# Performance work log

Measured on AMD Instinct MI355X. Metric: run time of the kernel, lower is better.

Reference implementation:

```python
import jax, jax.numpy as jnp
import numpy as np

B, L, H, NH = 32, 512, 256, 4
DH = H // NH
EPS = 1e-12


def setup_inputs() -> dict:
    key = jax.random.key(0)
    ks = jax.random.split(key, 24)
    p = lambda k, shape: 0.02 * jax.random.normal(k, shape, dtype=jnp.float32)
    return {
        "input_tensor": jax.random.normal(ks[0], (B, L, H), dtype=jnp.float32),
        # sorted positive timestamps (seconds-like scale)
        "time_seq": jnp.sort(jax.random.uniform(ks[1], (B, L), dtype=jnp.float32) * 100.0, axis=-1),
        "attention_mask": jnp.zeros((B, 1, L, L), dtype=jnp.float32),
        "item_seq_len": jnp.clip(jax.random.randint(ks[2], (B,), 0, L), 2, L),
        "Wq": p(ks[3], (H, H)), "bq": jnp.zeros((H,), jnp.float32),
        "Wk": p(ks[4], (H, H)), "bk": jnp.zeros((H,), jnp.float32),
        "Wv": p(ks[5], (H, H)), "bv": jnp.zeros((H,), jnp.float32),
        "Wd": p(ks[6], (H, H)), "bd": jnp.zeros((H,), jnp.float32),
        "ln_g": jnp.ones((H,), jnp.float32), "ln_b": jnp.zeros((H,), jnp.float32),
        "Wtq": p(ks[7], (H, H)), "btq": jnp.zeros((H,), jnp.float32),
        "tw1": p(ks[8], (L, L)), "tb1": p(ks[9], (L, L)),
        "tow1": p(ks[10], (L, L)), "tow2": p(ks[11], (L, L)), "tob": p(ks[12], (L, L)),
        "Wt": p(ks[13], (1, 2 * H)), "bt": jnp.zeros((1,), jnp.float32),
    }


def reference(input_tensor, time_seq, attention_mask, item_seq_len,
              Wq, bq, Wk, bk, Wv, bv, Wd, bd, ln_g, ln_b,
              Wtq, btq, tw1, tb1, tow1, tow2, tob, Wt, bt):
    x = input_tensor  # (B, L, H)

    def heads(t):  # (B,L,H) -> (B,NH,L,DH)
        return t.reshape(B, L, NH, DH).transpose(0, 2, 1, 3)

    q = heads(x @ Wq.T + bq)
    k = heads(x @ Wk.T + bk)
    v = heads(x @ Wv.T + bv)

    scores = jnp.einsum('bhqd,bhkd->bhqk', q, k)  # (B,NH,L,L)

    # --- time decay gate ---
    tq = x @ Wtq.T + btq                                  # (B,L,H)
    time_query_key = jnp.tanh(jnp.einsum('bqh,bkh->bqk', tq, x))  # (B,L,L)
    diff = jnp.abs(time_seq[:, :, None] - time_seq[:, None, :])   # |t_i - t_j|
    decay = jnp.tanh(jnp.log1p(diff) * tw1 + tb1)
    decay_gate = tow1 * decay + tow2 * time_query_key + tob       # (B,L,L)
    time_attn = jax.nn.sigmoid(decay_gate)[:, None, :, :]         # (B,1,L,L)

    scores = scores * time_attn / jnp.sqrt(jnp.float32(DH)) + attention_mask
    probs = jax.nn.softmax(scores, axis=-1)

    ctx = jnp.einsum('bhqk,bhkd->bhqd', probs, v)
    ctx = ctx.transpose(0, 2, 1, 3).reshape(B, L, H)

    hs = ctx @ Wd.T + bd + x
    mu = jnp.mean(hs, axis=-1, keepdims=True)
    var = jnp.var(hs, axis=-1, keepdims=True)
    hs = (hs - mu) / jnp.sqrt(var + EPS) * ln_g + ln_b   # (B,L,H)

    bidx = jnp.arange(B)
    emb1 = hs[bidx, item_seq_len - 1]  # (B,H)
    emb2 = hs[bidx, item_seq_len - 2]  # (B,H)
    pred_intervals = jnp.concatenate([emb1, emb2], axis=1) @ Wt.T + bt  # (B,1)
    return hs, pred_intervals
```

## Files before the change

### kernel.cpp

```cpp
#include <hip/hip_runtime.h>
#include <math.h>

#define Bn 32
#define Ln 512
#define Hn 256
#define NHn 4
#define DHn 64

typedef __attribute__((ext_vector_type(8))) short bf16x8;
typedef __attribute__((ext_vector_type(4))) float f32x4;
typedef unsigned int uint32;

__device__ __forceinline__ short f2b(float f) {
    union { float f; uint32 u; } v; v.f = f;
    uint32 r = (v.u + 0x7FFFu + ((v.u >> 16) & 1u)) >> 16;
    return (short)r;
}
__device__ __forceinline__ float b2f(short h) {
    union { uint32 u; float f; } v; v.u = ((uint32)(unsigned short)h) << 16;
    return v.f;
}
__device__ __forceinline__ float fast_tanh(float x) {
    float e = __expf(2.f * x);
    return 1.f - 2.f * __builtin_amdgcn_rcpf(e + 1.f);
}
__device__ __forceinline__ float fast_sigmoid(float x) {
    return __builtin_amdgcn_rcpf(1.f + __expf(-x));
}

__global__ __launch_bounds__(256) void conv_kernel(
    const float* __restrict__ x,
    const float* __restrict__ Wq, const float* __restrict__ Wk,
    const float* __restrict__ Wv, const float* __restrict__ Wtq,
    const float* __restrict__ Wd,
    short* __restrict__ xb, short* __restrict__ wb)
{
    const size_t NLH = (size_t)Bn * Ln * Hn;
    size_t i4 = ((size_t)blockIdx.x * 256 + threadIdx.x) * 4;
    if (i4 < NLH) {
        float4 v = *(const float4*)(x + i4);
        short4 o; o.x = f2b(v.x); o.y = f2b(v.y); o.z = f2b(v.z); o.w = f2b(v.w);
        *(short4*)(xb + i4) = o;
    } else {
        size_t off = i4 - NLH;
        int w = (int)(off >> 16);
        size_t wi = off & 65535;
        const float* src = (w == 0) ? Wq : (w == 1) ? Wk : (w == 2) ? Wv : (w == 3) ? Wtq : Wd;
        float4 v = *(const float4*)(src + wi);
        short4 o; o.x = f2b(v.x); o.y = f2b(v.y); o.z = f2b(v.z); o.w = f2b(v.w);
        *(short4*)(wb + off) = o;
    }
}

struct Acc { f32x4 t[4]; };

__device__ __forceinline__ void gemm_tile_64(
    const short* __restrict__ A,
    const short* __restrict__ Bm,
    int K, short* As, short* Bs, Acc& acc)
{
    const int tid = threadIdx.x;
    const int lane = tid & 63, w = tid >> 6;
    const int quad = lane >> 4, lm = lane & 15;
    const int srow = tid >> 3;
    const int slot = tid & 7;

    for (int k0 = 0; k0 < K; k0 += 64) {
        __syncthreads();
#pragma unroll
        for (int iss = 0; iss < 2; ++iss) {
            int r = srow + iss * 32;
            bf16x8 av = *(const bf16x8*)(A + (size_t)r * K + k0 + slot * 8);
            bf16x8 bv = *(const bf16x8*)(Bm + (size_t)r * K + k0 + slot * 8);
            *(bf16x8*)(As + r * 72 + slot * 8) = av;
            *(bf16x8*)(Bs + r * 72 + slot * 8) = bv;
        }
        __syncthreads();
#pragma unroll
        for (int ks = 0; ks < 2; ++ks) {
            bf16x8 a = *(const bf16x8*)(As + (w * 16 + lm) * 72 + ks * 32 + quad * 8);
#pragma unroll
            for (int kt = 0; kt < 4; ++kt) {
                bf16x8 b = *(const bf16x8*)(Bs + (kt * 16 + lm) * 72 + ks * 32 + quad * 8);
                acc.t[kt] = __builtin_amdgcn_mfma_f32_16x16x32_bf16(a, b, acc.t[kt], 0, 0, 0);
            }
        }
    }
}

__global__ __launch_bounds__(256) void proj_kernel(
    const short* __restrict__ xb, const short* __restrict__ wb,
    const float* __restrict__ bq, const float* __restrict__ bk,
    const float* __restrict__ bv, const float* __restrict__ btq,
    short* __restrict__ qb, short* __restrict__ kb,
    short* __restrict__ vt, short* __restrict__ tqb)
{
    __shared__ short As[64 * 72];
    __shared__ short Bs[64 * 72];
    const int bid = blockIdx.y * 16 + blockIdx.x;
    const int xcd = bid & 7, idx = bid >> 3;
    const int v = xcd * 512 + idx;
    const int tensor = (v & 15) >> 2;
    const int ncol0 = (v & 3) * 64;
    const int m0 = (v >> 4) * 64;
    const short* A = xb + (size_t)m0 * Hn;
    const short* Bw = wb + (size_t)tensor * 65536 + (size_t)ncol0 * Hn;
    const float* bias = (tensor == 0) ? bq : (tensor == 1) ? bk : (tensor == 2) ? bv : btq;

    Acc acc;
#pragma unroll
    for (int i = 0; i < 4; ++i) acc.t[i] = (f32x4){0.f, 0.f, 0.f, 0.f};
    gemm_tile_64(A, Bw, Hn, As, Bs, acc);

    const int lane = threadIdx.x & 63, w = threadIdx.x >> 6;
    const int quad = lane >> 4, lm = lane & 15;

    if (tensor == 2) {
#pragma unroll
        for (int kt = 0; kt < 4; ++kt) {
            int n = ncol0 + kt * 16 + lm;
            float bs = bv[n];
            int h = n >> 6, d = n & 63;
#pragma unroll
            for (int r = 0; r < 4; ++r) {
                int row = m0 + w * 16 + quad * 4 + r;
                int bb = row >> 9, l = row & 511;
                vt[((size_t)(bb * NHn + h) * DHn + d) * Ln + l] = f2b(acc.t[kt][r] + bs);
            }
        }
    } else {
        short* out = (tensor == 0) ? qb : (tensor == 1) ? kb : tqb;
#pragma unroll
        for (int kt = 0; kt < 4; ++kt) {
            int n = ncol0 + kt * 16 + lm;
            float bs = bias[n];
#pragma unroll
            for (int r = 0; r < 4; ++r) {
                int row = m0 + w * 16 + quad * 4 + r;
                out[(size_t)row * Hn + n] = f2b(acc.t[kt][r] + bs);
            }
        }
    }
}

__global__ __launch_bounds__(256) void gate_kernel(
    const short* __restrict__ tqb, const short* __restrict__ xb,
    const float* __restrict__ tseq,
    const float* __restrict__ tw1, const float* __restrict__ tb1,
    const float* __restrict__ tow1, const float* __restrict__ tow2,
    const float* __restrict__ tob,
    short* __restrict__ gateb)
{
    __shared__ short As[64 * 72];
    __shared__ short Bs[64 * 72];
    const int b = blockIdx.z;
    const int m0 = blockIdx.y * 64, n0 = blockIdx.x * 64;
    const short* A = tqb + ((size_t)b * Ln + m0) * Hn;
    const short* Bw = xb + ((size_t)b * Ln + n0) * Hn;

    Acc acc;
#pragma unroll
    for (int i = 0; i < 4; ++i) acc.t[i] = (f32x4){0.f, 0.f, 0.f, 0.f};
    gemm_tile_64(A, Bw, Hn, As, Bs, acc);

    const int tid = threadIdx.x;
    const int lane = tid & 63, w = tid >> 6;
    const int quad = lane >> 4, lm = lane & 15;
    const float* ts = tseq + (size_t)b * Ln;
    float ti[4];
#pragma unroll
    for (int r = 0; r < 4; ++r) ti[r] = ts[m0 + w * 16 + quad * 4 + r];

    bf16x8 g01, g23;
#pragma unroll
    for (int kt = 0; kt < 4; ++kt) {
        int j = n0 + kt * 16 + lm;
        float tj = ts[j];
#pragma unroll
        for (int r = 0; r < 4; ++r) {
            int i = m0 + w * 16 + quad * 4 + r;
            size_t ij = (size_t)i * Ln + j;
            float lg = __logf(1.f + fabsf(ti[r] - tj));
            float dec = fast_tanh(lg * tw1[ij] + tb1[ij]);
            float tqk = fast_tanh(acc.t[kt][r]);
            float dg = tow1[ij] * dec + tow2[ij] * tqk + tob[ij];
            float g = 0.125f * fast_sigmoid(dg);
            if (kt < 2) g01[kt * 4 + r] = f2b(g);
            else        g23[(kt - 2) * 4 + r] = f2b(g);
        }
    }
    size_t base = ((((size_t)b * 8 + blockIdx.y) * 8 + blockIdx.x) * 256 + tid) * 16;
    *(bf16x8*)(gateb + base) = g01;
    *(bf16x8*)(gateb + base + 8) = g23;
}

__global__ __launch_bounds__(256) void flash_mfma(
    const short* __restrict__ qb, const short* __restrict__ kb,
    const short* __restrict__ vt, const short* __restrict__ gateb,
    const float* __restrict__ mask, short* __restrict__ ctxb)
{
    __shared__ short Ks[64 * 72];
    __shared__ short Vt[64 * 72];
    __shared__ short Ps[4 * 16 * 72];
    const int mb = blockIdx.x;
    const int q0 = mb * 64;
    const int h = blockIdx.y, b = blockIdx.z;
    const int tid = threadIdx.x;
    const int w = tid >> 6, lane = tid & 63;
    const int quad = lane >> 4, lm = lane & 15;
    const int srow = tid >> 3, slot = tid & 7;

    bf16x8 qf0, qf1;
    {
        const short* qrow = qb + ((size_t)(b * Ln + q0 + w * 16 + lm)) * Hn + h * DHn;
        qf0 = *(const bf16x8*)(qrow + quad * 8);
        qf1 = *(const bf16x8*)(qrow + 32 + quad * 8);
    }

    f32x4 o[4];
#pragma unroll
    for (int i = 0; i < 4; ++i) o[i] = (f32x4){0.f, 0.f, 0.f, 0.f};
    float m_run[4] = {-INFINITY, -INFINITY, -INFINITY, -INFINITY};
    float l_run[4] = {0.f, 0.f, 0.f, 0.f};
    const float* mk_base = mask + (size_t)b * Ln * Ln;
    const int qrow0 = q0 + w * 16 + quad * 4;
    const short* kbase = kb + ((size_t)(b * Ln)) * Hn + h * DHn;
    const short* vbase = vt + (size_t)(b * NHn + h) * DHn * Ln;
    const short* gtile0 = gateb + (((size_t)b * 8 + mb) * 8 * 256 + tid) * 16;

    for (int k0 = 0; k0 < Ln; k0 += 64) {
        __syncthreads();
#pragma unroll
        for (int iss = 0; iss < 2; ++iss) {
            int r = srow + iss * 32;
            bf16x8 kv = *(const bf16x8*)(kbase + (size_t)(k0 + r) * Hn + slot * 8);
            bf16x8 vv = *(const bf16x8*)(vbase + (size_t)r * Ln + k0 + slot * 8);
            *(bf16x8*)(Ks + r * 72 + slot * 8) = kv;
            *(bf16x8*)(Vt + r * 72 + slot * 8) = vv;
        }
        __syncthreads();

        const short* gt = gtile0 + (size_t)(k0 >> 6) * 256 * 16;
        bf16x8 g01 = *(const bf16x8*)(gt);
        bf16x8 g23 = *(const bf16x8*)(gt + 8);
        float mvv[4][4];
#pragma unroll
        for (int kt = 0; kt < 4; ++kt) {
            int col = k0 + kt * 16 + lm;
#pragma unroll
            for (int r = 0; r < 4; ++r)
                mvv[kt][r] = mk_base[(size_t)(qrow0 + r) * Ln + col];
        }

        f32x4 s[4];
#pragma unroll
        for (int kt = 0; kt < 4; ++kt) {
            s[kt] = (f32x4){0.f, 0.f, 0.f, 0.f};
            bf16x8 b0 = *(const bf16x8*)(Ks + (kt * 16 + lm) * 72 + quad * 8);
            s[kt] = __builtin_amdgcn_mfma_f32_16x16x32_bf16(qf0, b0, s[kt], 0, 0, 0);
            bf16x8 b1 = *(const bf16x8*)(Ks + (kt * 16 + lm) * 72 + 32 + quad * 8);
            s[kt] = __builtin_amdgcn_mfma_f32_16x16x32_bf16(qf1, b1, s[kt], 0, 0, 0);
        }

        float mnew[4];
#pragma unroll
        for (int r = 0; r < 4; ++r) mnew[r] = m_run[r];
#pragma unroll
        for (int kt = 0; kt < 4; ++kt)
#pragma unroll
            for (int r = 0; r < 4; ++r) {
                float g = b2f(kt < 2 ? g01[(kt & 1) * 4 + r] : g23[(kt & 1) * 4 + r]);
                float sv = s[kt][r] * g + mvv[kt][r];
                s[kt][r] = sv;
                mnew[r] = fmaxf(mnew[r], sv);
            }
        float alpha[4], rsum[4];
#pragma unroll
        for (int r = 0; r < 4; ++r) {
#pragma unroll
            for (int off = 1; off < 16; off <<= 1)
                mnew[r] = fmaxf(mnew[r], __shfl_xor(mnew[r], off, 64));
            alpha[r] = __expf(m_run[r] - mnew[r]);
            m_run[r] = mnew[r];
            rsum[r] = 0.f;
        }
        float p[4][4];
#pragma unroll
        for (int kt = 0; kt < 4; ++kt)
#pragma unroll
            for (int r = 0; r < 4; ++r) {
                float pv = __expf(s[kt][r] - m_run[r]);
                p[kt][r] = pv;
                rsum[r] += pv;
            }
#pragma unroll
        for (int r = 0; r < 4; ++r) {
#pragma unroll
            for (int off = 1; off < 16; off <<= 1) rsum[r] += __shfl_xor(rsum[r], off, 64);
            l_run[r] = l_run[r] * alpha[r] + rsum[r];
#pragma unroll
            for (int ot = 0; ot < 4; ++ot) o[ot][r] *= alpha[r];
        }
        short* pw = Ps + w * 16 * 72;
#pragma unroll
        for (int kt = 0; kt < 4; ++kt)
#pragma unroll
            for (int r = 0; r < 4; ++r)
                pw[(quad * 4 + r) * 72 + kt * 16 + lm] = f2b(p[kt][r]);

#pragma unroll
        for (int ks = 0; ks < 2; ++ks) {
            bf16x8 pa = *(const bf16x8*)(pw + lm * 72 + ks * 32 + quad * 8);
#pragma unroll
            for (int ot = 0; ot < 4; ++ot) {
                bf16x8 vv = *(const bf16x8*)(Vt + (ot * 16 + lm) * 72 + ks * 32 + quad * 8);
                o[ot] = __builtin_amdgcn_mfma_f32_16x16x32_bf16(pa, vv, o[ot], 0, 0, 0);
            }
        }
    }

    float inv[4];
#pragma unroll
    for (int r = 0; r < 4; ++r) inv[r] = 1.0f / l_run[r];
#pragma unroll
    for (int ot = 0; ot < 4; ++ot) {
        int d = h * DHn + ot * 16 + lm;
#pragma unroll
        for (int r = 0; r < 4; ++r) {
            int row = b * Ln + qrow0 + r;
            ctxb[(size_t)row * Hn + d] = f2b(o[ot][r] * inv[r]);
        }
    }
}

__global__ __launch_bounds__(256) void outproj_ln_kernel(
    const short* __restrict__ ctxb, const short* __restrict__ wdb,
    const float* __restrict__ bd, const float* __restrict__ x,
    const float* __restrict__ g, const float* __restrict__ beta,
    float* __restrict__ out)
{
    const int m0 = blockIdx.x * 64;
    const int tid = threadIdx.x;
    const int lane = tid & 63, w = tid >> 6;
    const int quad = lane >> 4, lm = lane & 15;

    const short* arow = ctxb + (size_t)(m0 + w * 16 + lm) * Hn;
    bf16x8 af[8];
#pragma unroll
    for (int k8 = 0; k8 < 8; ++k8)
        af[k8] = *(const bf16x8*)(arow + k8 * 32 + quad * 8);

    f32x4 acc[4][4];
#pragma unroll
    for (int i = 0; i < 4; ++i)
#pragma unroll
        for (int j = 0; j < 4; ++j) acc[i][j] = (f32x4){0.f, 0.f, 0.f, 0.f};

#pragma unroll
    for (int k8 = 0; k8 < 8; ++k8) {
#pragma unroll
        for (int nt = 0; nt < 4; ++nt)
#pragma unroll
            for (int kt = 0; kt < 4; ++kt) {
                bf16x8 bf = *(const bf16x8*)(wdb + (size_t)(nt * 64 + kt * 16 + lm) * Hn + k8 * 32 + quad * 8);
                acc[nt][kt] = __builtin_amdgcn_mfma_f32_16x16x32_bf16(af[k8], bf, acc[nt][kt], 0, 0, 0);
            }
    }

    const int rl0 = w * 16 + quad * 4;
    float s1[4] = {0.f, 0.f, 0.f, 0.f}, s2[4] = {0.f, 0.f, 0.f, 0.f};
#pragma unroll
    for (int nt = 0; nt < 4; ++nt)
#pragma unroll
        for (int kt = 0; kt < 4; ++kt) {
            int col = nt * 64 + kt * 16 + lm;
            float bdv = bd[col];
#pragma unroll
            for (int r = 0; r < 4; ++r) {
                float xv = x[(size_t)(m0 + rl0 + r) * Hn + col];
                float hv = acc[nt][kt][r] + bdv + xv;
                acc[nt][kt][r] = hv;
                s1[r] += hv;
                s2[r] += hv * hv;
            }
        }
#pragma unroll
    for (int r = 0; r < 4; ++r) {
#pragma unroll
        for (int off = 1; off < 16; off <<= 1) {
            s1[r] += __shfl_xor(s1[r], off, 64);
            s2[r] += __shfl_xor(s2[r], off, 64);
        }
    }
    float mu[4], rstd[4];
#pragma unroll
    for (int r = 0; r < 4; ++r) {
        mu[r] = s1[r] * (1.f / 256.f);
        float var = s2[r] * (1.f / 256.f) - mu[r] * mu[r];
        rstd[r] = rsqrtf(var + 1e-12f);
    }
#pragma unroll
    for (int nt = 0; nt < 4; ++nt)
#pragma unroll
        for (int kt = 0; kt < 4; ++kt) {
            int col = nt * 64 + kt * 16 + lm;
            float gv = g[col], bb = beta[col];
#pragma unroll
            for (int r = 0; r < 4; ++r)
                out[(size_t)(m0 + rl0 + r) * Hn + col] =
                    (acc[nt][kt][r] - mu[r]) * rstd[r] * gv + bb;
        }
}

__global__ __launch_bounds__(256) void pred_kernel(const float* __restrict__ hs,
                                                   const int* __restrict__ lens,
                                                   const float* __restrict__ Wt,
                                                   const float* __restrict__ bt,
                                                   float* __restrict__ pred)
{
    const int b = blockIdx.x, t = threadIdx.x;
    int len = lens[b];
    float e1 = hs[((size_t)b * Ln + (len - 1)) * Hn + t];
    float e2 = hs[((size_t)b * Ln + (len - 2)) * Hn + t];
    float v = e1 * Wt[t] + e2 * Wt[Hn + t];
#pragma unroll
    for (int off = 32; off > 0; off >>= 1) v += __shfl_xor(v, off, 64);
    __shared__ float ps[4];
    if ((t & 63) == 0) ps[t >> 6] = v;
    __syncthreads();
    if (t == 0) pred[b] = ps[0] + ps[1] + ps[2] + ps[3] + bt[0];
}

extern "C" void kernel_launch(void* const* d_in, const int* in_sizes, int n_in,
                              void* d_out, int out_size, void* d_ws, size_t ws_size,
                              hipStream_t stream) {
    (void)in_sizes; (void)n_in; (void)out_size; (void)ws_size;
    const float* x    = (const float*)d_in[0];
    const float* tseq = (const float*)d_in[1];
    const float* mask = (const float*)d_in[2];
    const int*   lens = (const int*)d_in[3];
    const float* Wq = (const float*)d_in[4];  const float* bq = (const float*)d_in[5];
    const float* Wk = (const float*)d_in[6];  const float* bk = (const float*)d_in[7];
    const float* Wv = (const float*)d_in[8];  const float* bv = (const float*)d_in[9];
    const float* Wd = (const float*)d_in[10]; const float* bd = (const float*)d_in[11];
    const float* ln_g = (const float*)d_in[12]; const float* ln_b = (const float*)d_in[13];
    const float* Wtq = (const float*)d_in[14]; const float* btq = (const float*)d_in[15];
    const float* tw1 = (const float*)d_in[16]; const float* tb1 = (const float*)d_in[17];
    const float* tow1 = (const float*)d_in[18]; const float* tow2 = (const float*)d_in[19];
    const float* tob = (const float*)d_in[20];
    const float* Wt = (const float*)d_in[21]; const float* bt = (const float*)d_in[22];

    const size_t NLH = (size_t)Bn * Ln * Hn;
    short* ws = (short*)d_ws;
    short* xb    = ws;
    short* wb    = xb + NLH;
    short* qb    = wb + 5 * 65536;
    short* kb    = qb + NLH;
    short* vt    = kb + NLH;
    short* tqb   = vt + NLH;
    short* gateb = tqb + NLH;
    short* ctxb  = tqb;
    float* out   = (float*)d_out;

    dim3 blk(256);
    conv_kernel<<<dim3(4416), blk, 0, stream>>>(x, Wq, Wk, Wv, Wtq, Wd, xb, wb);
    proj_kernel<<<dim3(16, 256), blk, 0, stream>>>(xb, wb, bq, bk, bv, btq, qb, kb, vt, tqb);
    gate_kernel<<<dim3(8, 8, Bn), blk, 0, stream>>>(tqb, xb, tseq, tw1, tb1, tow1, tow2, tob, gateb);
    flash_mfma<<<dim3(8, NHn, Bn), blk, 0, stream>>>(qb, kb, vt, gateb, mask, ctxb);
    outproj_ln_kernel<<<dim3(256), blk, 0, stream>>>(ctxb, wb + 4 * 65536, bd, x, ln_g, ln_b, out);
    pred_kernel<<<dim3(Bn), blk, 0, stream>>>(out, lens, Wt, bt, out + NLH);
}
```

Baseline: 232.9 us.

## Pre-pack mask as bf16 interleaved with gate; split outproj+LN across more blocks

The fp32 attention mask is converted once to bf16 in the conversion kernel and stored interleaved with the gate tile, so each flash block reads gate and mask in one contiguous 64-byte chunk per thread. Before, every one of the 4 heads re-read the fp32 mask with scattered loads. The out-projection+LayerNorm kernel now processes 16 rows per block over 1024 blocks, with waves splitting the columns and an LDS reduction for the row statistics, which raises parallelism. Rounding the mask to bf16 changes precision, though the mask is zero here, and the gate buffer doubles in size.

```diff
diff --git a/kernel.cpp b/kernel.cpp
--- a/kernel.cpp
+++ b/kernel.cpp
@@ -32,23 +32,46 @@
     const float* __restrict__ x,
     const float* __restrict__ Wq, const float* __restrict__ Wk,
     const float* __restrict__ Wv, const float* __restrict__ Wtq,
-    const float* __restrict__ Wd,
-    short* __restrict__ xb, short* __restrict__ wb)
+    const float* __restrict__ Wd, const float* __restrict__ mask,
+    short* __restrict__ xb, short* __restrict__ wb, short* __restrict__ gmb)
 {
     const size_t NLH = (size_t)Bn * Ln * Hn;
-    size_t i4 = ((size_t)blockIdx.x * 256 + threadIdx.x) * 4;
-    if (i4 < NLH) {
-        float4 v = *(const float4*)(x + i4);
-        short4 o; o.x = f2b(v.x); o.y = f2b(v.y); o.z = f2b(v.z); o.w = f2b(v.w);
-        *(short4*)(xb + i4) = o;
+    const int bid = blockIdx.x;
+    if (bid < 4416) {
+        size_t i4 = ((size_t)bid * 256 + threadIdx.x) * 4;
+        if (i4 < NLH) {
+            float4 v = *(const float4*)(x + i4);
+            short4 o; o.x = f2b(v.x); o.y = f2b(v.y); o.z = f2b(v.z); o.w = f2b(v.w);
+            *(short4*)(xb + i4) = o;
+        } else {
+            size_t off = i4 - NLH;
+            int w = (int)(off >> 16);
+            size_t wi = off & 65535;
+            const float* src = (w == 0) ? Wq : (w == 1) ? Wk : (w == 2) ? Wv : (w == 3) ? Wtq : Wd;
+            float4 v = *(const float4*)(src + wi);
+            short4 o; o.x = f2b(v.x); o.y = f2b(v.y); o.z = f2b(v.z); o.w = f2b(v.w);
+            *(short4*)(wb + off) = o;
+        }
     } else {
-        size_t off = i4 - NLH;
-        int w = (int)(off >> 16);
-        size_t wi = off & 65535;
-        const float* src = (w == 0) ? Wq : (w == 1) ? Wk : (w == 2) ? Wv : (w == 3) ? Wtq : Wd;
-        float4 v = *(const float4*)(src + wi);
-        short4 o; o.x = f2b(v.x); o.y = f2b(v.y); o.z = f2b(v.z); o.w = f2b(v.w);
-        *(short4*)(wb + off) = o;
+        int off = bid - 4416;
+        int b = off >> 6, mb = (off >> 3) & 7, nb = off & 7;
+        int tid = threadIdx.x;
+        int i0 = mb * 64 + (tid >> 6) * 16 + ((tid >> 4) & 3) * 4;
+        const float* mbase = mask + (size_t)b * Ln * Ln;
+        bf16x8 m01, m23;
+#pragma unroll
+        for (int kt = 0; kt < 4; ++kt) {
+            int j = nb * 64 + kt * 16 + (tid & 15);
+#pragma unroll
+            for (int r = 0; r < 4; ++r) {
+                float mv = mbase[(size_t)(i0 + r) * Ln + j];
+                if (kt < 2) m01[kt * 4 + r] = f2b(mv);
+                else        m23[(kt - 2) * 4 + r] = f2b(mv);
+            }
+        }
+        size_t base = ((((size_t)b * 8 + mb) * 8 + nb) * 256 + tid) * 32;
+        *(bf16x8*)(gmb + base + 16) = m01;
+        *(bf16x8*)(gmb + base + 24) = m23;
     }
 }
 
@@ -149,7 +172,7 @@
     const float* __restrict__ tw1, const float* __restrict__ tb1,
     const float* __restrict__ tow1, const float* __restrict__ tow2,
     const float* __restrict__ tob,
-    short* __restrict__ gateb)
+    short* __restrict__ gmb)
 {
     __shared__ short As[64 * 72];
     __shared__ short Bs[64 * 72];
@@ -189,15 +212,15 @@
             else        g23[(kt - 2) * 4 + r] = f2b(g);
         }
     }
-    size_t base = ((((size_t)b * 8 + blockIdx.y) * 8 + blockIdx.x) * 256 + tid) * 16;
-    *(bf16x8*)(gateb + base) = g01;
-    *(bf16x8*)(gateb + base + 8) = g23;
+    size_t base = ((((size_t)b * 8 + blockIdx.y) * 8 + blockIdx.x) * 256 + tid) * 32;
+    *(bf16x8*)(gmb + base) = g01;
+    *(bf16x8*)(gmb + base + 8) = g23;
 }
 
 __global__ __launch_bounds__(256) void flash_mfma(
     const short* __restrict__ qb, const short* __restrict__ kb,
-    const short* __restrict__ vt, const short* __restrict__ gateb,
-    const float* __restrict__ mask, short* __restrict__ ctxb)
+    const short* __restrict__ vt, const short* __restrict__ gmb,
+    short* __restrict__ ctxb)
 {
     __shared__ short Ks[64 * 72];
     __shared__ short Vt[64 * 72];
@@ -222,11 +245,10 @@
     for (int i = 0; i < 4; ++i) o[i] = (f32x4){0.f, 0.f, 0.f, 0.f};
     float m_run[4] = {-INFINITY, -INFINITY, -INFINITY, -INFINITY};
     float l_run[4] = {0.f, 0.f, 0.f, 0.f};
-    const float* mk_base = mask + (size_t)b * Ln * Ln;
     const int qrow0 = q0 + w * 16 + quad * 4;
     const short* kbase = kb + ((size_t)(b * Ln)) * Hn + h * DHn;
     const short* vbase = vt + (size_t)(b * NHn + h) * DHn * Ln;
-    const short* gtile0 = gateb + (((size_t)b * 8 + mb) * 8 * 256 + tid) * 16;
+    const short* gm0 = gmb + (((size_t)b * 8 + mb) * 8 * 256 + tid) * 32;
 
     for (int k0 = 0; k0 < Ln; k0 += 64) {
         __syncthreads();
@@ -240,17 +262,11 @@
         }
         __syncthreads();
 
-        const short* gt = gtile0 + (size_t)(k0 >> 6) * 256 * 16;
-        bf16x8 g01 = *(const bf16x8*)(gt);
-        bf16x8 g23 = *(const bf16x8*)(gt + 8);
-        float mvv[4][4];
-#pragma unroll
-        for (int kt = 0; kt < 4; ++kt) {
-            int col = k0 + kt * 16 + lm;
-#pragma unroll
-            for (int r = 0; r < 4; ++r)
-                mvv[kt][r] = mk_base[(size_t)(qrow0 + r) * Ln + col];
-        }
+        const short* gm = gm0 + (size_t)(k0 >> 6) * 256 * 32;
+        bf16x8 g01 = *(const bf16x8*)(gm);
+        bf16x8 g23 = *(const bf16x8*)(gm + 8);
+        bf16x8 m01 = *(const bf16x8*)(gm + 16);
+        bf16x8 m23 = *(const bf16x8*)(gm + 24);
 
         f32x4 s[4];
 #pragma unroll
@@ -269,8 +285,9 @@
         for (int kt = 0; kt < 4; ++kt)
 #pragma unroll
             for (int r = 0; r < 4; ++r) {
-                float g = b2f(kt < 2 ? g01[(kt & 1) * 4 + r] : g23[(kt & 1) * 4 + r]);
-                float sv = s[kt][r] * g + mvv[kt][r];
+                float g  = b2f(kt < 2 ? g01[(kt & 1) * 4 + r] : g23[(kt & 1) * 4 + r]);
+                float mv = b2f(kt < 2 ? m01[(kt & 1) * 4 + r] : m23[(kt & 1) * 4 + r]);
+                float sv = s[kt][r] * g + mv;
                 s[kt][r] = sv;
                 mnew[r] = fmaxf(mnew[r], sv);
             }
@@ -339,77 +356,79 @@
     const float* __restrict__ g, const float* __restrict__ beta,
     float* __restrict__ out)
 {
-    const int m0 = blockIdx.x * 64;
+    const int m0 = blockIdx.x * 16;
     const int tid = threadIdx.x;
     const int lane = tid & 63, w = tid >> 6;
     const int quad = lane >> 4, lm = lane & 15;
 
-    const short* arow = ctxb + (size_t)(m0 + w * 16 + lm) * Hn;
+    const short* arow = ctxb + (size_t)(m0 + lm) * Hn;
     bf16x8 af[8];
 #pragma unroll
     for (int k8 = 0; k8 < 8; ++k8)
         af[k8] = *(const bf16x8*)(arow + k8 * 32 + quad * 8);
 
-    f32x4 acc[4][4];
-#pragma unroll
-    for (int i = 0; i < 4; ++i)
-#pragma unroll
-        for (int j = 0; j < 4; ++j) acc[i][j] = (f32x4){0.f, 0.f, 0.f, 0.f};
-
-#pragma unroll
-    for (int k8 = 0; k8 < 8; ++k8) {
-#pragma unroll
-        for (int nt = 0; nt < 4; ++nt)
-#pragma unroll
-            for (int kt = 0; kt < 4; ++kt) {
-                bf16x8 bf = *(const bf16x8*)(wdb + (size_t)(nt * 64 + kt * 16 + lm) * Hn + k8 * 32 + quad * 8);
-                acc[nt][kt] = __builtin_amdgcn_mfma_f32_16x16x32_bf16(af[k8], bf, acc[nt][kt], 0, 0, 0);
-            }
-    }
-
-    const int rl0 = w * 16 + quad * 4;
+    f32x4 acc[4];
+#pragma unroll
+    for (int i = 0; i < 4; ++i) acc[i] = (f32x4){0.f, 0.f, 0.f, 0.f};
+
+#pragma unroll
+    for (int k8 = 0; k8 < 8; ++k8)
+#pragma unroll
+        for (int kt = 0; kt < 4; ++kt) {
+            bf16x8 bf = *(const bf16x8*)(wdb + (size_t)(w * 64 + kt * 16 + lm) * Hn + k8 * 32 + quad * 8);
+            acc[kt] = __builtin_amdgcn_mfma_f32_16x16x32_bf16(af[k8], bf, acc[kt], 0, 0, 0);
+        }
+
     float s1[4] = {0.f, 0.f, 0.f, 0.f}, s2[4] = {0.f, 0.f, 0.f, 0.f};
 #pragma unroll
-    for (int nt = 0; nt < 4; ++nt)
-#pragma unroll
-        for (int kt = 0; kt < 4; ++kt) {
-            int col = nt * 64 + kt * 16 + lm;
-            float bdv = bd[col];
-#pragma unroll
-            for (int r = 0; r < 4; ++r) {
-                float xv = x[(size_t)(m0 + rl0 + r) * Hn + col];
-                float hv = acc[nt][kt][r] + bdv + xv;
-                acc[nt][kt][r] = hv;
-                s1[r] += hv;
-                s2[r] += hv * hv;
-            }
-        }
-#pragma unroll
-    for (int r = 0; r < 4; ++r) {
+    for (int kt = 0; kt < 4; ++kt) {
+        int col = w * 64 + kt * 16 + lm;
+        float bdv = bd[col];
+#pragma unroll
+        for (int r = 0; r < 4; ++r) {
+            int row = m0 + quad * 4 + r;
+            float xv = x[(size_t)row * Hn + col];
+            float hv = acc[kt][r] + bdv + xv;
+            acc[kt][r] = hv;
+            s1[r] += hv;
+            s2[r] += hv * hv;
+        }
+    }
+#pragma unroll
+    for (int r = 0; r < 4; ++r)
 #pragma unroll
         for (int off = 1; off < 16; off <<= 1) {
             s1[r] += __shfl_xor(s1[r], off, 64);
             s2[r] += __shfl_xor(s2[r], off, 64);
         }
-    }
+    __shared__ float red1[4][16], red2[4][16];
+    if (lm == 0) {
+#pragma unroll
+        for (int r = 0; r < 4; ++r) {
+            red1[w][quad * 4 + r] = s1[r];
+            red2[w][quad * 4 + r] = s2[r];
+        }
+    }
+    __syncthreads();
     float mu[4], rstd[4];
 #pragma unroll
     for (int r = 0; r < 4; ++r) {
-        mu[r] = s1[r] * (1.f / 256.f);
-        float var = s2[r] * (1.f / 256.f) - mu[r] * mu[r];
+        int row = quad * 4 + r;
+        float S1 = red1[0][row] + red1[1][row] + red1[2][row] + red1[3][row];
+        float S2 = red2[0][row] + red2[1][row] + red2[2][row] + red2[3][row];
+        mu[r] = S1 * (1.f / 256.f);
+        float var = S2 * (1.f / 256.f) - mu[r] * mu[r];
         rstd[r] = rsqrtf(var + 1e-12f);
     }
 #pragma unroll
-    for (int nt = 0; nt < 4; ++nt)
-#pragma unroll
-        for (int kt = 0; kt < 4; ++kt) {
-            int col = nt * 64 + kt * 16 + lm;
-            float gv = g[col], bb = beta[col];
-#pragma unroll
-            for (int r = 0; r < 4; ++r)
-                out[(size_t)(m0 + rl0 + r) * Hn + col] =
-                    (acc[nt][kt][r] - mu[r]) * rstd[r] * gv + bb;
-        }
+    for (int kt = 0; kt < 4; ++kt) {
+        int col = w * 64 + kt * 16 + lm;
+        float gv = g[col], bb = beta[col];
+#pragma unroll
+        for (int r = 0; r < 4; ++r)
+            out[(size_t)(m0 + quad * 4 + r) * Hn + col] =
+                (acc[kt][r] - mu[r]) * rstd[r] * gv + bb;
+    }
 }
 
 __global__ __launch_bounds__(256) void pred_kernel(const float* __restrict__ hs,
@@ -458,15 +477,15 @@
     short* kb    = qb + NLH;
     short* vt    = kb + NLH;
     short* tqb   = vt + NLH;
-    short* gateb = tqb + NLH;
+    short* gmb   = tqb + NLH;
     short* ctxb  = tqb;
     float* out   = (float*)d_out;
 
     dim3 blk(256);
-    conv_kernel<<<dim3(4416), blk, 0, stream>>>(x, Wq, Wk, Wv, Wtq, Wd, xb, wb);
+    conv_kernel<<<dim3(6464), blk, 0, stream>>>(x, Wq, Wk, Wv, Wtq, Wd, mask, xb, wb, gmb);
     proj_kernel<<<dim3(16, 256), blk, 0, stream>>>(xb, wb, bq, bk, bv, btq, qb, kb, vt, tqb);
-    gate_kernel<<<dim3(8, 8, Bn), blk, 0, stream>>>(tqb, xb, tseq, tw1, tb1, tow1, tow2, tob, gateb);
-    flash_mfma<<<dim3(8, NHn, Bn), blk, 0, stream>>>(qb, kb, vt, gateb, mask, ctxb);
-    outproj_ln_kernel<<<dim3(256), blk, 0, stream>>>(ctxb, wb + 4 * 65536, bd, x, ln_g, ln_b, out);
+    gate_kernel<<<dim3(8, 8, Bn), blk, 0, stream>>>(tqb, xb, tseq, tw1, tb1, tow1, tow2, tob, gmb);
+    flash_mfma<<<dim3(8, NHn, Bn), blk, 0, stream>>>(qb, kb, vt, gmb, ctxb);
+    outproj_ln_kernel<<<dim3(1024), blk, 0, stream>>>(ctxb, wb + 4 * 65536, bd, x, ln_g, ln_b, out);
     pred_kernel<<<dim3(Bn), blk, 0, stream>>>(out, lens, Wt, bt, out + NLH);
 }
```

Result: slower. 253.2 us (+8.7%).

## Fuse time-query projection into gate kernel and pred into outproj-LN

Applied to the files above, without the earlier changes.

Merges the gate computation with the Wtq projection. The gate blocks compute tq for their 64-row tile into LDS and use it directly as the A operand of the tq·x^T GEMM, so tq is never written to or reread from global memory. The QKV projection tiles share the same launch as extra blocks. The prediction head moves into the output-projection/LayerNorm kernel via atomicAdd, with pred initialized to bt in the conversion kernel. This removes two launches and a global round trip, but the gate blocks now do redundant tq work (each m-tile computed twice across the nh halves) and read B fragments straight from global memory without LDS staging.

```diff
diff --git a/kernel.cpp b/kernel.cpp
--- a/kernel.cpp
+++ b/kernel.cpp
@@ -32,10 +32,11 @@
     const float* __restrict__ x,
     const float* __restrict__ Wq, const float* __restrict__ Wk,
     const float* __restrict__ Wv, const float* __restrict__ Wtq,
-    const float* __restrict__ Wd,
-    short* __restrict__ xb, short* __restrict__ wb)
+    const float* __restrict__ Wd, const float* __restrict__ bt,
+    short* __restrict__ xb, short* __restrict__ wb, float* __restrict__ pred)
 {
     const size_t NLH = (size_t)Bn * Ln * Hn;
+    if (blockIdx.x == 0 && threadIdx.x < Bn) pred[threadIdx.x] = bt[0];
     size_t i4 = ((size_t)blockIdx.x * 256 + threadIdx.x) * 4;
     if (i4 < NLH) {
         float4 v = *(const float4*)(x + i4);
@@ -88,110 +89,148 @@
     }
 }
 
-__global__ __launch_bounds__(256) void proj_kernel(
+__global__ __launch_bounds__(256) void projgate_kernel(
     const short* __restrict__ xb, const short* __restrict__ wb,
     const float* __restrict__ bq, const float* __restrict__ bk,
     const float* __restrict__ bv, const float* __restrict__ btq,
-    short* __restrict__ qb, short* __restrict__ kb,
-    short* __restrict__ vt, short* __restrict__ tqb)
-{
-    __shared__ short As[64 * 72];
-    __shared__ short Bs[64 * 72];
-    const int bid = blockIdx.y * 16 + blockIdx.x;
-    const int xcd = bid & 7, idx = bid >> 3;
-    const int v = xcd * 512 + idx;
-    const int tensor = (v & 15) >> 2;
-    const int ncol0 = (v & 3) * 64;
-    const int m0 = (v >> 4) * 64;
-    const short* A = xb + (size_t)m0 * Hn;
-    const short* Bw = wb + (size_t)tensor * 65536 + (size_t)ncol0 * Hn;
-    const float* bias = (tensor == 0) ? bq : (tensor == 1) ? bk : (tensor == 2) ? bv : btq;
-
-    Acc acc;
-#pragma unroll
-    for (int i = 0; i < 4; ++i) acc.t[i] = (f32x4){0.f, 0.f, 0.f, 0.f};
-    gemm_tile_64(A, Bw, Hn, As, Bs, acc);
-
-    const int lane = threadIdx.x & 63, w = threadIdx.x >> 6;
-    const int quad = lane >> 4, lm = lane & 15;
-
-    if (tensor == 2) {
-#pragma unroll
-        for (int kt = 0; kt < 4; ++kt) {
-            int n = ncol0 + kt * 16 + lm;
-            float bs = bv[n];
-            int h = n >> 6, d = n & 63;
-#pragma unroll
-            for (int r = 0; r < 4; ++r) {
-                int row = m0 + w * 16 + quad * 4 + r;
-                int bb = row >> 9, l = row & 511;
-                vt[((size_t)(bb * NHn + h) * DHn + d) * Ln + l] = f2b(acc.t[kt][r] + bs);
-            }
-        }
-    } else {
-        short* out = (tensor == 0) ? qb : (tensor == 1) ? kb : tqb;
-#pragma unroll
-        for (int kt = 0; kt < 4; ++kt) {
-            int n = ncol0 + kt * 16 + lm;
-            float bs = bias[n];
-#pragma unroll
-            for (int r = 0; r < 4; ++r) {
-                int row = m0 + w * 16 + quad * 4 + r;
-                out[(size_t)row * Hn + n] = f2b(acc.t[kt][r] + bs);
-            }
-        }
-    }
-}
-
-__global__ __launch_bounds__(256) void gate_kernel(
-    const short* __restrict__ tqb, const short* __restrict__ xb,
     const float* __restrict__ tseq,
     const float* __restrict__ tw1, const float* __restrict__ tb1,
     const float* __restrict__ tow1, const float* __restrict__ tow2,
     const float* __restrict__ tob,
-    short* __restrict__ gateb)
+    short* __restrict__ qb, short* __restrict__ kb,
+    short* __restrict__ vt, short* __restrict__ gateb)
 {
-    __shared__ short As[64 * 72];
-    __shared__ short Bs[64 * 72];
-    const int b = blockIdx.z;
-    const int m0 = blockIdx.y * 64, n0 = blockIdx.x * 64;
-    const short* A = tqb + ((size_t)b * Ln + m0) * Hn;
-    const short* Bw = xb + ((size_t)b * Ln + n0) * Hn;
-
-    Acc acc;
-#pragma unroll
-    for (int i = 0; i < 4; ++i) acc.t[i] = (f32x4){0.f, 0.f, 0.f, 0.f};
-    gemm_tile_64(A, Bw, Hn, As, Bs, acc);
-
+    __shared__ short lds[64 * 264];
+    const int bid = blockIdx.x;
     const int tid = threadIdx.x;
     const int lane = tid & 63, w = tid >> 6;
     const int quad = lane >> 4, lm = lane & 15;
-    const float* ts = tseq + (size_t)b * Ln;
-    float ti[4];
-#pragma unroll
-    for (int r = 0; r < 4; ++r) ti[r] = ts[m0 + w * 16 + quad * 4 + r];
-
-    bf16x8 g01, g23;
-#pragma unroll
-    for (int kt = 0; kt < 4; ++kt) {
-        int j = n0 + kt * 16 + lm;
-        float tj = ts[j];
-#pragma unroll
-        for (int r = 0; r < 4; ++r) {
-            int i = m0 + w * 16 + quad * 4 + r;
-            size_t ij = (size_t)i * Ln + j;
-            float lg = __logf(1.f + fabsf(ti[r] - tj));
-            float dec = fast_tanh(lg * tw1[ij] + tb1[ij]);
-            float tqk = fast_tanh(acc.t[kt][r]);
-            float dg = tow1[ij] * dec + tow2[ij] * tqk + tob[ij];
-            float g = 0.125f * fast_sigmoid(dg);
-            if (kt < 2) g01[kt * 4 + r] = f2b(g);
-            else        g23[(kt - 2) * 4 + r] = f2b(g);
-        }
-    }
-    size_t base = ((((size_t)b * 8 + blockIdx.y) * 8 + blockIdx.x) * 256 + tid) * 16;
-    *(bf16x8*)(gateb + base) = g01;
-    *(bf16x8*)(gateb + base + 8) = g23;
+
+    if (bid < 512) {
+        const int b = bid >> 4;
+        const int mtile = (bid >> 1) & 7, nh = bid & 1;
+        const int m0 = mtile * 64;
+        const short* xrow_base = xb + (size_t)b * Ln * Hn;
+
+        const short* arow = xrow_base + (size_t)(m0 + w * 16 + lm) * Hn;
+        bf16x8 af[8];
+#pragma unroll
+        for (int k8 = 0; k8 < 8; ++k8)
+            af[k8] = *(const bf16x8*)(arow + k8 * 32 + quad * 8);
+        const short* wtq = wb + 3 * 65536;
+#pragma unroll
+        for (int nc = 0; nc < 4; ++nc) {
+            f32x4 acc1[4];
+#pragma unroll
+            for (int i = 0; i < 4; ++i) acc1[i] = (f32x4){0.f, 0.f, 0.f, 0.f};
+#pragma unroll
+            for (int k8 = 0; k8 < 8; ++k8)
+#pragma unroll
+                for (int kt = 0; kt < 4; ++kt) {
+                    bf16x8 bf = *(const bf16x8*)(wtq + (size_t)(nc * 64 + kt * 16 + lm) * Hn + k8 * 32 + quad * 8);
+                    acc1[kt] = __builtin_amdgcn_mfma_f32_16x16x32_bf16(af[k8], bf, acc1[kt], 0, 0, 0);
+                }
+#pragma unroll
+            for (int kt = 0; kt < 4; ++kt) {
+                int col = nc * 64 + kt * 16 + lm;
+                float bv_ = btq[col];
+#pragma unroll
+                for (int r = 0; r < 4; ++r)
+                    lds[(w * 16 + quad * 4 + r) * 264 + col] = f2b(acc1[kt][r] + bv_);
+            }
+        }
+        __syncthreads();
+
+        bf16x8 a2[8];
+#pragma unroll
+        for (int k8 = 0; k8 < 8; ++k8)
+            a2[k8] = *(const bf16x8*)(lds + (w * 16 + lm) * 264 + k8 * 32 + quad * 8);
+
+        const float* ts = tseq + (size_t)b * Ln;
+        float ti[4];
+#pragma unroll
+        for (int r = 0; r < 4; ++r) ti[r] = ts[m0 + w * 16 + quad * 4 + r];
+
+#pragma unroll
+        for (int nt4 = 0; nt4 < 4; ++nt4) {
+            const int nb = nh * 4 + nt4;
+            const int n0 = nb * 64;
+            f32x4 acc2[4];
+#pragma unroll
+            for (int i = 0; i < 4; ++i) acc2[i] = (f32x4){0.f, 0.f, 0.f, 0.f};
+#pragma unroll
+            for (int k8 = 0; k8 < 8; ++k8)
+#pragma unroll
+                for (int kt = 0; kt < 4; ++kt) {
+                    bf16x8 bf = *(const bf16x8*)(xrow_base + (size_t)(n0 + kt * 16 + lm) * Hn + k8 * 32 + quad * 8);
+                    acc2[kt] = __builtin_amdgcn_mfma_f32_16x16x32_bf16(a2[k8], bf, acc2[kt], 0, 0, 0);
+                }
+            bf16x8 g01, g23;
+#pragma unroll
+            for (int kt = 0; kt < 4; ++kt) {
+                int j = n0 + kt * 16 + lm;
+                float tj = ts[j];
+#pragma unroll
+                for (int r = 0; r < 4; ++r) {
+                    int i = m0 + w * 16 + quad * 4 + r;
+                    size_t ij = (size_t)i * Ln + j;
+                    float lg = __logf(1.f + fabsf(ti[r] - tj));
+                    float dec = fast_tanh(lg * tw1[ij] + tb1[ij]);
+                    float tqk = fast_tanh(acc2[kt][r]);
+                    float dg = tow1[ij] * dec + tow2[ij] * tqk + tob[ij];
+                    float gv = 0.125f * fast_sigmoid(dg);
+                    if (kt < 2) g01[kt * 4 + r] = f2b(gv);
+                    else        g23[(kt - 2) * 4 + r] = f2b(gv);
+                }
+            }
+            size_t base = ((((size_t)b * 8 + mtile) * 8 + nb) * 256 + tid) * 16;
+            *(bf16x8*)(gateb + base) = g01;
+            *(bf16x8*)(gateb + base + 8) = g23;
+        }
+    } else {
+        const int p = bid - 512;
+        const int xcd = p & 7, idx = p >> 3;
+        const int v = xcd * 384 + idx;
+        const int tv = v % 12;
+        const int tensor = tv >> 2;
+        const int ncol0 = (tv & 3) * 64;
+        const int m0 = (v / 12) * 64;
+        const short* A = xb + (size_t)m0 * Hn;
+        const short* Bw = wb + (size_t)tensor * 65536 + (size_t)ncol0 * Hn;
+        const float* bias = (tensor == 0) ? bq : (tensor == 1) ? bk : bv;
+
+        Acc acc;
+#pragma unroll
+        for (int i = 0; i < 4; ++i) acc.t[i] = (f32x4){0.f, 0.f, 0.f, 0.f};
+        gemm_tile_64(A, Bw, Hn, lds, lds + 64 * 72, acc);
+
+        if (tensor == 2) {
+#pragma unroll
+            for (int kt = 0; kt < 4; ++kt) {
+                int n = ncol0 + kt * 16 + lm;
+                float bs = bv[n];
+                int h = n >> 6, d = n & 63;
+#pragma unroll
+                for (int r = 0; r < 4; ++r) {
+                    int row = m0 + w * 16 + quad * 4 + r;
+                    int bb = row >> 9, l = row & 511;
+                    vt[((size_t)(bb * NHn + h) * DHn + d) * Ln + l] = f2b(acc.t[kt][r] + bs);
+                }
+            }
+        } else {
+            short* out = (tensor == 0) ? qb : kb;
+#pragma unroll
+            for (int kt = 0; kt < 4; ++kt) {
+                int n = ncol0 + kt * 16 + lm;
+                float bs = bias[n];
+#pragma unroll
+                for (int r = 0; r < 4; ++r) {
+                    int row = m0 + w * 16 + quad * 4 + r;
+                    out[(size_t)row * Hn + n] = f2b(acc.t[kt][r] + bs);
+                }
+            }
+        }
+    }
 }
 
 __global__ __launch_bounds__(256) void flash_mfma(
@@ -337,7 +376,8 @@
     const short* __restrict__ ctxb, const short* __restrict__ wdb,
     const float* __restrict__ bd, const float* __restrict__ x,
     const float* __restrict__ g, const float* __restrict__ beta,
-    float* __restrict__ out)
+    const int* __restrict__ lens, const float* __restrict__ Wt,
+    float* __restrict__ out, float* __restrict__ pred)
 {
     const int m0 = blockIdx.x * 64;
     const int tid = threadIdx.x;
@@ -399,36 +439,40 @@
         float var = s2[r] * (1.f / 256.f) - mu[r] * mu[r];
         rstd[r] = rsqrtf(var + 1e-12f);
     }
+
+    const int bb = m0 >> 9;
+    const int len = lens[bb];
+    const int loc1 = (bb << 9) + len - 1;
+    const int loc2 = loc1 - 1;
+    const bool own1 = (loc1 >= m0) && (loc1 < m0 + 64);
+    const bool own2 = (loc2 >= m0) && (loc2 < m0 + 64);
+    const bool active = own1 || own2;
+    float pacc = 0.f;
+
 #pragma unroll
     for (int nt = 0; nt < 4; ++nt)
 #pragma unroll
         for (int kt = 0; kt < 4; ++kt) {
             int col = nt * 64 + kt * 16 + lm;
-            float gv = g[col], bb = beta[col];
-#pragma unroll
-            for (int r = 0; r < 4; ++r)
-                out[(size_t)(m0 + rl0 + r) * Hn + col] =
-                    (acc[nt][kt][r] - mu[r]) * rstd[r] * gv + bb;
-        }
-}
-
-__global__ __launch_bounds__(256) void pred_kernel(const float* __restrict__ hs,
-                                                   const int* __restrict__ lens,
-                                                   const float* __restrict__ Wt,
-                                                   const float* __restrict__ bt,
-                                                   float* __restrict__ pred)
-{
-    const int b = blockIdx.x, t = threadIdx.x;
-    int len = lens[b];
-    float e1 = hs[((size_t)b * Ln + (len - 1)) * Hn + t];
-    float e2 = hs[((size_t)b * Ln + (len - 2)) * Hn + t];
-    float v = e1 * Wt[t] + e2 * Wt[Hn + t];
-#pragma unroll
-    for (int off = 32; off > 0; off >>= 1) v += __shfl_xor(v, off, 64);
-    __shared__ float ps[4];
-    if ((t & 63) == 0) ps[t >> 6] = v;
-    __syncthreads();
-    if (t == 0) pred[b] = ps[0] + ps[1] + ps[2] + ps[3] + bt[0];
+            float gv = g[col], bb2 = beta[col];
+            float wt1 = 0.f, wt2 = 0.f;
+            if (active) { wt1 = Wt[col]; wt2 = Wt[Hn + col]; }
+#pragma unroll
+            for (int r = 0; r < 4; ++r) {
+                int row = m0 + rl0 + r;
+                float val = (acc[nt][kt][r] - mu[r]) * rstd[r] * gv + bb2;
+                out[(size_t)row * Hn + col] = val;
+                if (active) {
+                    if (row == loc1) pacc += val * wt1;
+                    else if (row == loc2) pacc += val * wt2;
+                }
+            }
+        }
+    if (active) {
+#pragma unroll
+        for (int off = 1; off < 64; off <<= 1) pacc += __shfl_xor(pacc, off, 64);
+        if (lane == 0) atomicAdd(&pred[bb], pacc);
+    }
 }
 
 extern "C" void kernel_launch(void* const* d_in, const int* in_sizes, int n_in,
@@ -457,16 +501,17 @@
     short* qb    = wb + 5 * 65536;
     short* kb    = qb + NLH;
     short* vt    = kb + NLH;
-    short* tqb   = vt + NLH;
-    short* gateb = tqb + NLH;
-    short* ctxb  = tqb;
+    short* gateb = vt + NLH;
+    short* ctxb  = gateb + (size_t)Bn * Ln * Ln;
     float* out   = (float*)d_out;
+    float* pred  = out + NLH;
 
     dim3 blk(256);
-    conv_kernel<<<dim3(4416), blk, 0, stream>>>(x, Wq, Wk, Wv, Wtq, Wd, xb, wb);
-    proj_kernel<<<dim3(16, 256), blk, 0, stream>>>(xb, wb, bq, bk, bv, btq, qb, kb, vt, tqb);
-    gate_kernel<<<dim3(8, 8, Bn), blk, 0, stream>>>(tqb, xb, tseq, tw1, tb1, tow1, tow2, tob, gateb);
+    conv_kernel<<<dim3(4416), blk, 0, stream>>>(x, Wq, Wk, Wv, Wtq, Wd, bt, xb, wb, pred);
+    projgate_kernel<<<dim3(3584), blk, 0, stream>>>(xb, wb, bq, bk, bv, btq, tseq,
+                                                    tw1, tb1, tow1, tow2, tob,
+                                                    qb, kb, vt, gateb);
     flash_mfma<<<dim3(8, NHn, Bn), blk, 0, stream>>>(qb, kb, vt, gateb, mask, ctxb);
-    outproj_ln_kernel<<<dim3(256), blk, 0, stream>>>(ctxb, wb + 4 * 65536, bd, x, ln_g, ln_b, out);
-    pred_kernel<<<dim3(Bn), blk, 0, stream>>>(out, lens, Wt, bt, out + NLH);
-}
+    outproj_ln_kernel<<<dim3(256), blk, 0, stream>>>(ctxb, wb + 4 * 65536, bd, x,
+                                                     ln_g, ln_b, lens, Wt, out, pred);
+}
```

Measured after the change: 278.9 us. 1.2x slower.
